# Optimization experiments

Hardware: AMD Instinct MI355X
Metric: run time of the kernel (lower is better)

The kernel has to match this reference:

```python
import jax, jax.numpy as jnp
import numpy as np
import math

N_HEADS = 8
INPUT_DIM = 128
EMBED_DIM = 128
KEY_DIM = 16
VAL_DIM = 16
BATCH = 2
SEQ = 4096


def setup_inputs() -> dict:
    key = jax.random.key(0)
    kq, kh, km, k1, k2, k3, k4 = jax.random.split(key, 7)
    q = jax.random.normal(kq, (BATCH, SEQ, INPUT_DIM), dtype=jnp.float32)
    h = jax.random.normal(kh, (BATCH, SEQ, INPUT_DIM), dtype=jnp.float32)
    mask = jax.random.randint(km, (BATCH, SEQ, SEQ), 0, 2).astype(jnp.bool_)
    # uniform(-stdv, stdv) with stdv = 1/sqrt(last_dim), matching init_parameters()
    def uni(k, shape):
        stdv = 1.0 / math.sqrt(shape[-1])
        return jax.random.uniform(k, shape, jnp.float32, -stdv, stdv)
    W_query = uni(k1, (N_HEADS, INPUT_DIM, KEY_DIM))
    W_key = uni(k2, (N_HEADS, INPUT_DIM, KEY_DIM))
    W_val = uni(k3, (N_HEADS, INPUT_DIM, VAL_DIM))
    W_out = uni(k4, (N_HEADS, VAL_DIM, EMBED_DIM))
    return {"q": q, "h": h, "mask": mask, "W_query": W_query,
            "W_key": W_key, "W_val": W_val, "W_out": W_out}


def reference(q, h, mask, W_query, W_key, W_val, W_out):
    norm = 1.0 / math.sqrt(KEY_DIM)
    # per-head projections: (h,b,n,k)
    Q = jnp.einsum('bni,hik->hbnk', q, W_query)
    K = jnp.einsum('bmi,hik->hbmk', h, W_key)
    V = jnp.einsum('bmi,hiv->hbmv', h, W_val)
    # full dense score tensor (h,b,n,m) — matches original materialization
    compat = norm * jnp.einsum('hbnk,hbmk->hbnm', Q, K)
    m = mask[None]  # broadcast over heads
    compat = jnp.where(m, -jnp.inf, compat)
    attn = jax.nn.softmax(compat, axis=-1)
    attn = jnp.where(m, 0.0, attn)
    heads = jnp.einsum('hbnm,hbmv->hbnv', attn, V)
    out = jnp.einsum('hbnv,hve->bne', heads, W_out)
    return out
```

## Files before the change

kernel.cpp:

```cpp
#include <hip/hip_runtime.h>
#include <stdint.h>

#define SEQ 4096
#define DIM 128
#define NHEADS 8
#define HDK 16

typedef __bf16 bf16x2 __attribute__((ext_vector_type(2)));
typedef __bf16 bf16x8 __attribute__((ext_vector_type(8)));
typedef float f32x16 __attribute__((ext_vector_type(16)));
typedef float f32x4 __attribute__((ext_vector_type(4)));
typedef unsigned uint2v __attribute__((ext_vector_type(2)));
typedef unsigned uint4v __attribute__((ext_vector_type(4)));

__device__ inline unsigned short f2bf(float x) {
  unsigned u = __builtin_bit_cast(unsigned, x);
  u = (u + 0x7FFFu + ((u >> 16) & 1u)) >> 16;
  return (unsigned short)u;
}
__device__ inline unsigned pkbf(float lo, float hi) {
  return (unsigned)f2bf(lo) | ((unsigned)f2bf(hi) << 16);
}
__device__ inline unsigned pkbf_fast(float lo, float hi) {
  bf16x2 t;
  t[0] = (__bf16)lo;
  t[1] = (__bf16)hi;
  return __builtin_bit_cast(unsigned, t);
}
__device__ inline float fexp2(float x) {
#if __has_builtin(__builtin_amdgcn_exp2f)
  return __builtin_amdgcn_exp2f(x);
#else
  return exp2f(x);
#endif
}
__device__ inline float apply_keep(float e, unsigned mrs, int kvc) {
#if __has_builtin(__builtin_amdgcn_sbfe)
  const unsigned m = (unsigned)__builtin_amdgcn_sbfe((int)mrs, kvc, 1);
#else
  const unsigned m = (unsigned)(((int)(mrs << (31 - kvc))) >> 31);
#endif
  return __builtin_bit_cast(float, __builtin_bit_cast(unsigned, e) & ~m);
}

__global__ __launch_bounds__(256) void k_mask(
    const void* __restrict__ maskp, unsigned* __restrict__ bits,
    unsigned* __restrict__ Vt32w) {
  const int tid = threadIdx.x;
  if (blockIdx.x >= 512) {
    const int base = (int)(blockIdx.x - 512) * 256 + tid;
    #pragma unroll
    for (int j = 0; j < 32; ++j) {
      const int w = base + j * 1024;
      const int bh = w >> 11;
      const int n2 = w & 2047;
      Vt32w[((size_t)bh * 32 + 16) * 2048 + n2] = 0x3F803F80u;
    }
    return;
  }
  __shared__ unsigned lds[128][17];
  const unsigned*      mw = (const unsigned*)maskp;
  const unsigned char* m8 = (const unsigned char*)maskp;
  bool wordmode = true;
  #pragma unroll
  for (int i = 0; i < 32; ++i) {
    unsigned w = mw[i];
    if (!(w == 0u || w == 1u || w == 0x3F800000u)) wordmode = false;
  }
  const int b = (int)(blockIdx.x >> 8);
  const int rowbase = (int)(blockIdx.x & 255) * 16;
  const int kt = tid & 127;
  #pragma unroll
  for (int p = 0; p < 8; ++p) {
    const int rl = p * 2 + (tid >> 7);
    const size_t g = ((size_t)b * SEQ + rowbase + rl) * SEQ + kt * 32;
    unsigned word = 0;
    if (wordmode) {
      uint4v w0 = *(const uint4v*)(mw + g);
      uint4v w1 = *(const uint4v*)(mw + g + 4);
      uint4v w2 = *(const uint4v*)(mw + g + 8);
      uint4v w3 = *(const uint4v*)(mw + g + 12);
      uint4v w4 = *(const uint4v*)(mw + g + 16);
      uint4v w5 = *(const uint4v*)(mw + g + 20);
      uint4v w6 = *(const uint4v*)(mw + g + 24);
      uint4v w7 = *(const uint4v*)(mw + g + 28);
      const uint4v wv[8] = { w0, w1, w2, w3, w4, w5, w6, w7 };
      #pragma unroll
      for (int j = 0; j < 8; ++j)
        #pragma unroll
        for (int e = 0; e < 4; ++e) {
          const unsigned w = wv[j][e];
          word |= ((w | (0u - w)) >> 31) << (4 * j + e);
        }
    } else {
      uint4v c0 = *(const uint4v*)(m8 + g);
      uint4v c1 = *(const uint4v*)(m8 + g + 16);
      const uint4v cv[2] = { c0, c1 };
      #pragma unroll
      for (int j = 0; j < 2; ++j)
        #pragma unroll
        for (int e = 0; e < 4; ++e) {
          unsigned w = cv[j][e];
          #pragma unroll
          for (int by = 0; by < 4; ++by) {
            word |= ((w & 0xFFu) ? 1u : 0u) << (16 * j + 4 * e + by);
            w >>= 8;
          }
        }
    }
    lds[kt][rl] = word;
  }
  __syncthreads();
  #pragma unroll
  for (int j = 0; j < 8; ++j) {
    const int idx = tid + 256 * j;
    const int k2 = idx >> 4, rl = idx & 15;
    bits[((size_t)b * 128 + k2) * SEQ + rowbase + rl] = lds[k2][rl];
  }
}

__global__ __launch_bounds__(256) void k_proj(
    const float* __restrict__ qin, const float* __restrict__ hin,
    const float* __restrict__ Wq, const float* __restrict__ Wk, const float* __restrict__ Wv,
    unsigned short* __restrict__ Qp, unsigned short* __restrict__ Kp,
    unsigned short* __restrict__ Vt32) {
  __shared__ float Wl[128][128];
  __shared__ float inl[8][128];
  const int mat = blockIdx.y;
  const float* in = (mat == 0) ? qin : hin;
  const float* W  = (mat == 0) ? Wq : (mat == 1 ? Wk : Wv);
  for (int e = threadIdx.x; e < 128 * 128; e += 256) {
    int i = e >> 7, c = e & 127;
    Wl[i][c] = W[((size_t)((c >> 4) * 128 + i)) * 16 + (c & 15)];
  }
  const int r  = threadIdx.x >> 5;
  const int cg = (threadIdx.x & 31) << 2;
  const size_t rb = (size_t)blockIdx.x * 64;
  const float SCALE_Q = 0.25f * 1.4426950408889634f;
  for (int pass = 0; pass < 8; ++pass) {
    __syncthreads();
    size_t row0 = rb + pass * 8;
    for (int e = threadIdx.x; e < 8 * 128; e += 256)
      inl[e >> 7][e & 127] = in[(row0 + (e >> 7)) * 128 + (e & 127)];
    __syncthreads();
    f32x4 acc = {0.f, 0.f, 0.f, 0.f};
    #pragma unroll 8
    for (int i = 0; i < 128; ++i) {
      float a = inl[r][i];
      acc += a * *(const f32x4*)&Wl[i][cg];
    }
    size_t grow = row0 + r;
    if (mat == 0) {
      uint2v o = { pkbf(acc[0] * SCALE_Q, acc[1] * SCALE_Q),
                   pkbf(acc[2] * SCALE_Q, acc[3] * SCALE_Q) };
      *(uint2v*)(Qp + grow * DIM + cg) = o;
    } else if (mat == 1) {
      uint2v o = { pkbf(acc[0], acc[1]), pkbf(acc[2], acc[3]) };
      *(uint2v*)(Kp + grow * DIM + cg) = o;
    } else {
      size_t b = grow >> 12, n = grow & 4095;
      #pragma unroll
      for (int j = 0; j < 4; ++j) {
        const int c = cg + j;
        Vt32[((size_t)(b * 8 + (c >> 4)) * 32 + (c & 15)) * SEQ + n] =
            f2bf(acc[j]);
      }
    }
  }
}

__global__ __launch_bounds__(512, 4) void k_flash(
    const unsigned short* __restrict__ Qp, const unsigned short* __restrict__ Kp,
    const unsigned short* __restrict__ Vt32, const unsigned* __restrict__ bits,
    float* __restrict__ parts, float* __restrict__ Lb, int NT) {
  const int tid  = threadIdx.x;
  const int wv   = tid >> 6;
  const int lane = tid & 63;
  const int q    = lane & 31;
  const int hi   = lane >> 5;
  const int h    = wv;
  const int sp   = blockIdx.x >> 8;
  const int bqb  = blockIdx.x & 255;
  const int b    = bqb >> 7;
  const int qb   = (bqb & 127) << 5;
  const int kt0  = sp * NT;

  const bf16x8 qfrag =
      *(const bf16x8*)(Qp + ((size_t)b * SEQ + qb + q) * DIM + h * HDK + hi * 8);
  const unsigned short* kbase =
      Kp + ((size_t)b * SEQ) * DIM + h * HDK + hi * 8 + (size_t)q * DIM;
  const int qv = q < 16 ? q : 16;
  const unsigned short* vbase =
      Vt32 + ((size_t)(b * 8 + h) * 32 + qv) * SEQ + hi * 8;
  const unsigned* bq = bits + ((size_t)b * 128 + kt0) * SEQ + qb + q;

  int koff = (kt0 << 5) * DIM;
  int boff = 0;
  int voff = kt0 << 5;

  unsigned mr0 = bq[0], mr1 = bq[SEQ];
  bf16x8 kf0 = *(const bf16x8*)(kbase + koff);
  bf16x8 kf1 = *(const bf16x8*)(kbase + koff + 32 * DIM);

  f32x16 oacc = {};
  const int niter = NT >> 1;

  for (int t = 0; t < niter; ++t) {
    f32x16 z16 = {};
    f32x16 st0 = __builtin_amdgcn_mfma_f32_32x32x16_bf16(kf0, qfrag, z16, 0, 0, 0);
    f32x16 st1 = __builtin_amdgcn_mfma_f32_32x32x16_bf16(kf1, qfrag, z16, 0, 0, 0);

    const int adv = (t + 1 < niter) ? 1 : 0;
    const unsigned mrn0 = bq[boff + adv * 2 * SEQ];
    const unsigned mrn1 = bq[boff + adv * 2 * SEQ + SEQ];
    const bf16x8 kfn0 = *(const bf16x8*)(kbase + koff + adv * 64 * DIM);
    const bf16x8 kfn1 = *(const bf16x8*)(kbase + koff + adv * 64 * DIM + 32 * DIM);

    const unsigned mrs0 = mr0 >> (hi << 2);
    const unsigned mrs1 = mr1 >> (hi << 2);

    #pragma unroll
    for (int T = 0; T < 2; ++T) {
      const unsigned mrs = T ? mrs1 : mrs0;
      #pragma unroll
      for (int sl = 0; sl < 2; ++sl) {
        float pe[8];
        #pragma unroll
        for (int j = 0; j < 8; ++j) {
          const int r = sl * 8 + j;
          const int kvc = (r & 3) + 8 * (r >> 2);
          pe[j] = apply_keep(fexp2(T ? st1[r] : st0[r]), mrs, kvc);
        }
        const unsigned a0 = pkbf_fast(pe[0], pe[1]);
        const unsigned a1 = pkbf_fast(pe[2], pe[3]);
        const unsigned b0 = pkbf_fast(pe[4], pe[5]);
        const unsigned b1 = pkbf_fast(pe[6], pe[7]);
        const uint2v s0 = __builtin_amdgcn_permlane32_swap(a0, b0, false, false);
        const uint2v s1 = __builtin_amdgcn_permlane32_swap(a1, b1, false, false);
        const uint4v w = { s0.x, s1.x, s0.y, s1.y };
        const bf16x8 pfrag = __builtin_bit_cast(bf16x8, w);
        const bf16x8 vf = *(const bf16x8*)(vbase + voff + T * 32 + sl * 16);
        oacc = __builtin_amdgcn_mfma_f32_32x32x16_bf16(vf, pfrag, oacc, 0, 0, 0);
      }
    }
    kf0 = kfn0; kf1 = kfn1; mr0 = mrn0; mr1 = mrn1;
    koff += adv * 64 * DIM;
    boff += adv * 2 * SEQ;
    voff += 64;
  }

  const size_t row = (size_t)b * SEQ + qb + q;
  float* hp = parts + ((size_t)sp * 2 * SEQ + row) * DIM + h * HDK;
  f32x4 w0 = { oacc[0], oacc[1], oacc[2], oacc[3] };
  f32x4 w1 = { oacc[4], oacc[5], oacc[6], oacc[7] };
  *(f32x4*)(hp + 4 * hi)     = w0;
  *(f32x4*)(hp + 8 + 4 * hi) = w1;
  if (hi == 0)
    Lb[((size_t)sp * 2 * SEQ + row) * NHEADS + h] = oacc[8];
}

__global__ __launch_bounds__(256) void k_oproj(
    const float* __restrict__ parts, const float* __restrict__ Lb,
    const float* __restrict__ Wo, float* __restrict__ out, int NS) {
  __shared__ float Wl[128][128];
  __shared__ float inl[8][128];
  for (int e = threadIdx.x; e < 128 * 128; e += 256) Wl[e >> 7][e & 127] = Wo[e];
  const int r  = threadIdx.x >> 5;
  const int cg = (threadIdx.x & 31) << 2;
  const int h  = cg >> 4;
  const size_t R  = (size_t)2 * SEQ;
  const size_t rb = (size_t)blockIdx.x * 32;
  for (int pass = 0; pass < 4; ++pass) {
    __syncthreads();
    const size_t row = rb + pass * 8 + r;
    float l = 0.f;
    f32x4 acc = {0.f, 0.f, 0.f, 0.f};
    for (int sp = 0; sp < NS; ++sp) {
      l += Lb[(sp * R + row) * NHEADS + h];
      acc += *(const f32x4*)&parts[(sp * R + row) * DIM + cg];
    }
    const float rinv = l > 0.f ? 1.0f / l : 0.f;
    *(f32x4*)&inl[r][cg] = acc * rinv;
    __syncthreads();
    f32x4 o = {0.f, 0.f, 0.f, 0.f};
    #pragma unroll 8
    for (int i = 0; i < 128; ++i) o += inl[r][i] * *(const f32x4*)&Wl[i][cg];
    *(f32x4*)(out + row * 128 + cg) = o;
  }
}

extern "C" void kernel_launch(void* const* d_in, const int* in_sizes, int n_in,
                              void* d_out, int out_size, void* d_ws, size_t ws_size,
                              hipStream_t stream) {
  const float* qin = (const float*)d_in[0];
  const float* hin = (const float*)d_in[1];
  const void* mask = d_in[2];
  const float* Wq  = (const float*)d_in[3];
  const float* Wk  = (const float*)d_in[4];
  const float* Wv  = (const float*)d_in[5];
  const float* Wo  = (const float*)d_in[6];
  float* out = (float*)d_out;
  char* ws = (char*)d_ws;

  const size_t MAT   = (size_t)2 * SEQ * DIM;
  const size_t VMAT  = (size_t)16 * 32 * SEQ;
  const size_t R     = (size_t)2 * SEQ;
  const size_t BITS  = (size_t)2 * 128 * SEQ;

  int NS = 4;
  while (NS > 1) {
    size_t need = 2 * MAT * 2 + VMAT * 2 + BITS * 4 +
                  (size_t)NS * (R * DIM * 4 + R * NHEADS * 4);
    if (need <= ws_size) break;
    NS >>= 1;
  }
  const int NT = 128 / NS;

  unsigned short* Qp    = (unsigned short*)ws;
  unsigned short* Kp    = Qp + MAT;
  unsigned short* Vt32  = Kp + MAT;
  unsigned*       bits  = (unsigned*)(Vt32 + VMAT);
  float*          parts = (float*)(bits + BITS);
  float*          Lb    = parts + (size_t)NS * R * DIM;

  k_proj<<<dim3(128, 3), 256, 0, stream>>>(qin, hin, Wq, Wk, Wv, Qp, Kp, Vt32);
  k_mask<<<516, 256, 0, stream>>>(mask, bits, (unsigned*)Vt32);
  k_flash<<<256 * NS, 512, 0, stream>>>(Qp, Kp, Vt32, bits, parts, Lb, NT);
  k_oproj<<<256, 256, 0, stream>>>(parts, Lb, Wo, out, NS);
}
```

Before: 151.7 us.

## Merge projection and mask kernels, split flash blocks into half-head groups

Combines the projection kernel and the mask bit-packing kernel into one launch, with block ranges selecting the role and the mask transpose reusing the projection LDS buffer. This removes one kernel launch and lets the two independent jobs run concurrently. The flash kernel now uses 256-thread blocks covering four heads each, with twice as many blocks and a higher occupancy hint, giving finer scheduling granularity across CUs. The trade-off is that each 32-row query tile now reads its mask bits twice, once per head group.

```diff
diff --git a/kernel.cpp b/kernel.cpp
--- a/kernel.cpp
+++ b/kernel.cpp
@@ -43,104 +43,109 @@
   return __builtin_bit_cast(float, __builtin_bit_cast(unsigned, e) & ~m);
 }
 
-__global__ __launch_bounds__(256) void k_mask(
-    const void* __restrict__ maskp, unsigned* __restrict__ bits,
-    unsigned* __restrict__ Vt32w) {
+__global__ __launch_bounds__(256) void k_pre(
+    const float* __restrict__ qin, const float* __restrict__ hin,
+    const float* __restrict__ Wq, const float* __restrict__ Wk,
+    const float* __restrict__ Wv, const void* __restrict__ maskp,
+    unsigned short* __restrict__ Qp, unsigned short* __restrict__ Kp,
+    unsigned short* __restrict__ Vt32, unsigned* __restrict__ bits) {
+  __shared__ float Wl[128][128];
+  __shared__ float inl[8][128];
+  const int bid = (int)blockIdx.x;
   const int tid = threadIdx.x;
-  if (blockIdx.x >= 512) {
-    const int base = (int)(blockIdx.x - 512) * 256 + tid;
+
+  if (bid >= 896) {
+    unsigned* Vt32w = (unsigned*)Vt32;
+    const int base = (bid - 896) * 256 + tid;
     #pragma unroll
     for (int j = 0; j < 32; ++j) {
       const int w = base + j * 1024;
-      const int bh = w >> 11;
-      const int n2 = w & 2047;
+      const int bh = w >> 11, n2 = w & 2047;
       Vt32w[((size_t)bh * 32 + 16) * 2048 + n2] = 0x3F803F80u;
     }
     return;
   }
-  __shared__ unsigned lds[128][17];
-  const unsigned*      mw = (const unsigned*)maskp;
-  const unsigned char* m8 = (const unsigned char*)maskp;
-  bool wordmode = true;
-  #pragma unroll
-  for (int i = 0; i < 32; ++i) {
-    unsigned w = mw[i];
-    if (!(w == 0u || w == 1u || w == 0x3F800000u)) wordmode = false;
-  }
-  const int b = (int)(blockIdx.x >> 8);
-  const int rowbase = (int)(blockIdx.x & 255) * 16;
-  const int kt = tid & 127;
-  #pragma unroll
-  for (int p = 0; p < 8; ++p) {
-    const int rl = p * 2 + (tid >> 7);
-    const size_t g = ((size_t)b * SEQ + rowbase + rl) * SEQ + kt * 32;
-    unsigned word = 0;
-    if (wordmode) {
-      uint4v w0 = *(const uint4v*)(mw + g);
-      uint4v w1 = *(const uint4v*)(mw + g + 4);
-      uint4v w2 = *(const uint4v*)(mw + g + 8);
-      uint4v w3 = *(const uint4v*)(mw + g + 12);
-      uint4v w4 = *(const uint4v*)(mw + g + 16);
-      uint4v w5 = *(const uint4v*)(mw + g + 20);
-      uint4v w6 = *(const uint4v*)(mw + g + 24);
-      uint4v w7 = *(const uint4v*)(mw + g + 28);
-      const uint4v wv[8] = { w0, w1, w2, w3, w4, w5, w6, w7 };
-      #pragma unroll
-      for (int j = 0; j < 8; ++j)
+
+  if (bid >= 384) {
+    unsigned (*mlds)[17] = (unsigned (*)[17])Wl;
+    const unsigned*      mw = (const unsigned*)maskp;
+    const unsigned char* m8 = (const unsigned char*)maskp;
+    bool wordmode = true;
+    #pragma unroll
+    for (int i = 0; i < 32; ++i) {
+      unsigned w = mw[i];
+      if (!(w == 0u || w == 1u || w == 0x3F800000u)) wordmode = false;
+    }
+    const int mb = bid - 384;
+    const int b = mb >> 8;
+    const int rowbase = (mb & 255) * 16;
+    const int kt = tid & 127;
+    #pragma unroll
+    for (int p = 0; p < 8; ++p) {
+      const int rl = p * 2 + (tid >> 7);
+      const size_t g = ((size_t)b * SEQ + rowbase + rl) * SEQ + kt * 32;
+      unsigned word = 0;
+      if (wordmode) {
+        uint4v w0 = *(const uint4v*)(mw + g);
+        uint4v w1 = *(const uint4v*)(mw + g + 4);
+        uint4v w2 = *(const uint4v*)(mw + g + 8);
+        uint4v w3 = *(const uint4v*)(mw + g + 12);
+        uint4v w4 = *(const uint4v*)(mw + g + 16);
+        uint4v w5 = *(const uint4v*)(mw + g + 20);
+        uint4v w6 = *(const uint4v*)(mw + g + 24);
+        uint4v w7 = *(const uint4v*)(mw + g + 28);
+        const uint4v wv[8] = { w0, w1, w2, w3, w4, w5, w6, w7 };
         #pragma unroll
-        for (int e = 0; e < 4; ++e) {
-          const unsigned w = wv[j][e];
-          word |= ((w | (0u - w)) >> 31) << (4 * j + e);
-        }
-    } else {
-      uint4v c0 = *(const uint4v*)(m8 + g);
-      uint4v c1 = *(const uint4v*)(m8 + g + 16);
-      const uint4v cv[2] = { c0, c1 };
-      #pragma unroll
-      for (int j = 0; j < 2; ++j)
+        for (int j = 0; j < 8; ++j)
+          #pragma unroll
+          for (int e = 0; e < 4; ++e) {
+            const unsigned w = wv[j][e];
+            word |= ((w | (0u - w)) >> 31) << (4 * j + e);
+          }
+      } else {
+        uint4v c0 = *(const uint4v*)(m8 + g);
+        uint4v c1 = *(const uint4v*)(m8 + g + 16);
+        const uint4v cv[2] = { c0, c1 };
         #pragma unroll
-        for (int e = 0; e < 4; ++e) {
-          unsigned w = cv[j][e];
+        for (int j = 0; j < 2; ++j)
           #pragma unroll
-          for (int by = 0; by < 4; ++by) {
-            word |= ((w & 0xFFu) ? 1u : 0u) << (16 * j + 4 * e + by);
-            w >>= 8;
+          for (int e = 0; e < 4; ++e) {
+            unsigned w = cv[j][e];
+            #pragma unroll
+            for (int by = 0; by < 4; ++by) {
+              word |= ((w & 0xFFu) ? 1u : 0u) << (16 * j + 4 * e + by);
+              w >>= 8;
+            }
           }
-        }
-    }
-    lds[kt][rl] = word;
-  }
-  __syncthreads();
-  #pragma unroll
-  for (int j = 0; j < 8; ++j) {
-    const int idx = tid + 256 * j;
-    const int k2 = idx >> 4, rl = idx & 15;
-    bits[((size_t)b * 128 + k2) * SEQ + rowbase + rl] = lds[k2][rl];
-  }
-}
-
-__global__ __launch_bounds__(256) void k_proj(
-    const float* __restrict__ qin, const float* __restrict__ hin,
-    const float* __restrict__ Wq, const float* __restrict__ Wk, const float* __restrict__ Wv,
-    unsigned short* __restrict__ Qp, unsigned short* __restrict__ Kp,
-    unsigned short* __restrict__ Vt32) {
-  __shared__ float Wl[128][128];
-  __shared__ float inl[8][128];
-  const int mat = blockIdx.y;
+      }
+      mlds[kt][rl] = word;
+    }
+    __syncthreads();
+    #pragma unroll
+    for (int j = 0; j < 8; ++j) {
+      const int idx = tid + 256 * j;
+      const int k2 = idx >> 4, rl = idx & 15;
+      bits[((size_t)b * 128 + k2) * SEQ + rowbase + rl] = mlds[k2][rl];
+    }
+    return;
+  }
+
+  const int mat = bid >> 7;
+  const int xb  = bid & 127;
   const float* in = (mat == 0) ? qin : hin;
   const float* W  = (mat == 0) ? Wq : (mat == 1 ? Wk : Wv);
-  for (int e = threadIdx.x; e < 128 * 128; e += 256) {
+  for (int e = tid; e < 128 * 128; e += 256) {
     int i = e >> 7, c = e & 127;
     Wl[i][c] = W[((size_t)((c >> 4) * 128 + i)) * 16 + (c & 15)];
   }
-  const int r  = threadIdx.x >> 5;
-  const int cg = (threadIdx.x & 31) << 2;
-  const size_t rb = (size_t)blockIdx.x * 64;
+  const int r  = tid >> 5;
+  const int cg = (tid & 31) << 2;
+  const size_t rb = (size_t)xb * 64;
   const float SCALE_Q = 0.25f * 1.4426950408889634f;
   for (int pass = 0; pass < 8; ++pass) {
     __syncthreads();
     size_t row0 = rb + pass * 8;
-    for (int e = threadIdx.x; e < 8 * 128; e += 256)
+    for (int e = tid; e < 8 * 128; e += 256)
       inl[e >> 7][e & 127] = in[(row0 + (e >> 7)) * 128 + (e & 127)];
     __syncthreads();
     f32x4 acc = {0.f, 0.f, 0.f, 0.f};
@@ -169,7 +174,7 @@
   }
 }
 
-__global__ __launch_bounds__(512, 4) void k_flash(
+__global__ __launch_bounds__(256, 8) void k_flash(
     const unsigned short* __restrict__ Qp, const unsigned short* __restrict__ Kp,
     const unsigned short* __restrict__ Vt32, const unsigned* __restrict__ bits,
     float* __restrict__ parts, float* __restrict__ Lb, int NT) {
@@ -178,11 +183,11 @@
   const int lane = tid & 63;
   const int q    = lane & 31;
   const int hi   = lane >> 5;
-  const int h    = wv;
-  const int sp   = blockIdx.x >> 8;
-  const int bqb  = blockIdx.x & 255;
+  const int h    = ((blockIdx.x & 1) << 2) + wv;
+  const int bqb  = (blockIdx.x >> 1) & 255;
   const int b    = bqb >> 7;
   const int qb   = (bqb & 127) << 5;
+  const int sp   = blockIdx.x >> 9;
   const int kt0  = sp * NT;
 
   const bf16x8 qfrag =
@@ -323,8 +328,7 @@
   float*          parts = (float*)(bits + BITS);
   float*          Lb    = parts + (size_t)NS * R * DIM;
 
-  k_proj<<<dim3(128, 3), 256, 0, stream>>>(qin, hin, Wq, Wk, Wv, Qp, Kp, Vt32);
-  k_mask<<<516, 256, 0, stream>>>(mask, bits, (unsigned*)Vt32);
-  k_flash<<<256 * NS, 512, 0, stream>>>(Qp, Kp, Vt32, bits, parts, Lb, NT);
+  k_pre<<<900, 256, 0, stream>>>(qin, hin, Wq, Wk, Wv, mask, Qp, Kp, Vt32, bits);
+  k_flash<<<512 * NS, 256, 0, stream>>>(Qp, Kp, Vt32, bits, parts, Lb, NT);
   k_oproj<<<256, 256, 0, stream>>>(parts, Lb, Wo, out, NS);
 }
```

New measurement: 172.9 us. 14.0% more time.
